# Optimization experiments

Hardware: AMD Instinct MI355X
Metric: run time of the kernel (lower is better)

Reference implementation:

```python
import math
import jax, jax.numpy as jnp
import numpy as np

EMBED_DIM = 1024
NUM_HEADS = 16
HEAD_DIM = EMBED_DIM // NUM_HEADS


def setup_inputs() -> dict:
    key = jax.random.key(0)
    kx, kqkv, kproj = jax.random.split(key, 3)
    b, sq, h = 2, 2048, EMBED_DIM
    x = jax.random.normal(kx, (b, sq, h), dtype=jnp.float32)
    # torch Linear weights are [out_features, in_features]
    # xavier_uniform for qkv: bound = sqrt(6/(fan_in+fan_out))
    bound_qkv = math.sqrt(6.0 / (h + 3 * h))
    Wqkv = jax.random.uniform(kqkv, (3 * h, h), dtype=jnp.float32,
                              minval=-bound_qkv, maxval=bound_qkv)
    # kaiming_uniform(a=sqrt(5)) for proj: bound = 1/sqrt(fan_in)
    bound_p = 1.0 / math.sqrt(h)
    Wproj = jax.random.uniform(kproj, (h, h), dtype=jnp.float32,
                               minval=-bound_p, maxval=bound_p)
    bproj = jnp.zeros((h,), dtype=jnp.float32)
    # self-attention: query == key == value (module asserts equality)
    return {"query": x, "key": x, "value": x,
            "Wqkv": Wqkv, "Wproj": Wproj, "bproj": bproj}


def reference(query, key, value, Wqkv, Wproj, bproj):
    b, sq, h = query.shape
    nh, hn = NUM_HEADS, HEAD_DIM
    # permute to [sq, b, h] then flatten tokens (seq-major)
    x = jnp.transpose(query, (1, 0, 2)).reshape(sq * b, h)
    qkv = x @ Wqkv.T                       # [sq*b, 3h] (no qkv bias: add_bias_kv=False)
    qkv = qkv.reshape(sq, b, nh, 3 * hn)
    q, k, v = jnp.split(qkv, 3, axis=-1)   # each [sq, b, nh, hn]
    # view to (sq, b*nh, hn) then transpose(0,1) -> [b*nh, sq, hn] (b-major, nh-minor)
    q = q.reshape(sq, b * nh, hn).transpose(1, 0, 2)
    k = k.reshape(sq, b * nh, hn).transpose(1, 0, 2)
    v = v.reshape(sq, b * nh, hn).transpose(1, 0, 2)
    scale = 1.0 / math.sqrt(hn)
    scores = jnp.einsum('nqd,nkd->nqk', q, k) * scale   # [b*nh, sq, sq] full matrix
    attn = jax.nn.softmax(scores, axis=-1)
    ctx = jnp.einsum('nqk,nkd->nqd', attn, v)           # [b*nh, sq, hn]
    # NOTE: original code views the b*nh (b-major) dim as (nh, b) -- reproduce exactly
    ctx = ctx.reshape(nh, b, sq, hn)
    ctx = jnp.transpose(ctx, (2, 1, 0, 3)).reshape(sq * b, h)
    out = ctx @ Wproj.T + bproj
    out = out.reshape(sq, b, h)
    return jnp.transpose(out, (1, 0, 2))   # [b, sq, h]
```

## Files before the change

### kernel.cpp

```cpp
#include <hip/hip_runtime.h>
#include <stdint.h>

#define B_   2
#define SQ   2048
#define H    1024
#define NH   16
#define HN   64
#define T_TOK 4096
#define N3H  3072

typedef __bf16 bf16x8 __attribute__((ext_vector_type(8)));
typedef float  f32x4  __attribute__((ext_vector_type(4)));
typedef float  f32x16 __attribute__((ext_vector_type(16)));

#define MFMA16(a, b, c) __builtin_amdgcn_mfma_f32_16x16x32_bf16((a), (b), (c), 0, 0, 0)
#define MFMA32(a, b, c) __builtin_amdgcn_mfma_f32_32x32x16_bf16((a), (b), (c), 0, 0, 0)

#define LGKM_DRAIN() do { \
  __builtin_amdgcn_s_waitcnt(0xC07F); \
  __builtin_amdgcn_wave_barrier(); \
} while (0)

__device__ __forceinline__ uint16_t f2bf_u(float f) {
  union { float f; uint32_t u; } v; v.f = f;
  uint32_t u = v.u;
  u += 0x7fffu + ((u >> 16) & 1u);
  return (uint16_t)(u >> 16);
}

__device__ __forceinline__ uint32_t cvtpk2(float a, float b, float* sum) {
  union { __bf16 h[2]; uint32_t u; } r;
  r.h[0] = (__bf16)a;
  r.h[1] = (__bf16)b;
  *sum += (float)r.h[0] + (float)r.h[1];
  return r.u;
}

__device__ __forceinline__ bf16x8 ldb8(const uint16_t* p) {
  return *reinterpret_cast<const bf16x8*>(p);
}

__device__ __forceinline__ void gll16(const uint16_t* g, uint16_t* l) {
  __builtin_amdgcn_global_load_lds(
      (const __attribute__((address_space(1))) uint32_t*)g,
      (__attribute__((address_space(3))) uint32_t*)l, 16, 0, 0);
}

__global__ __launch_bounds__(256) void convert_kernel(
    const float* __restrict__ x, const float* __restrict__ wqkv,
    const float* __restrict__ wproj,
    uint16_t* __restrict__ xb, uint16_t* __restrict__ wqkvb,
    uint16_t* __restrict__ wprojb) {
  const int XT4 = (T_TOK * H) / 4;
  const int WQ4 = (N3H * H) / 4;
  int i4 = blockIdx.x * 256 + threadIdx.x;
  const float* src;
  uint16_t* dst;
  if (i4 < XT4) {
    int i = i4 * 4;
    int t = i >> 10, c = i & 1023;
    int bi = t & 1, s = t >> 1;
    src = x + (bi * SQ + s) * H + c;
    dst = xb + i;
  } else if (i4 < XT4 + WQ4) {
    int j = (i4 - XT4) * 4;
    src = wqkv + j; dst = wqkvb + j;
  } else {
    int j = (i4 - XT4 - WQ4) * 4;
    src = wproj + j; dst = wprojb + j;
  }
  float4 v = *(const float4*)src;
  ushort4 o;
  o.x = f2bf_u(v.x); o.y = f2bf_u(v.y); o.z = f2bf_u(v.z); o.w = f2bf_u(v.w);
  *(ushort4*)dst = o;
}

__global__ __launch_bounds__(256) void gemm_qkv_kernel(
    const uint16_t* __restrict__ xb, const uint16_t* __restrict__ wb,
    uint16_t* __restrict__ Qb, uint16_t* __restrict__ Kb,
    uint16_t* __restrict__ Vtb) {
  const int lane = threadIdx.x & 63;
  const int wave = threadIdx.x >> 6;
  const int quad = lane >> 4, l16 = lane & 15;
  const int wm = wave >> 1, wn = wave & 1;
  const int row0 = blockIdx.y * 128, col0 = blockIdx.x * 128;

  __shared__ __align__(16) char smem[4 * 64 * 76 * 2];
  uint16_t* sA = (uint16_t*)smem;
  uint16_t* sB = (uint16_t*)(smem + 8192);
  uint16_t* W  = (uint16_t*)(smem) + wave * (64 * 76);

  const int lrow = lane >> 2;
  const int lk   = (lane & 3) * 8;

  f32x4 acc[4][4];
#pragma unroll
  for (int i = 0; i < 4; ++i)
#pragma unroll
    for (int j = 0; j < 4; ++j) acc[i][j] = (f32x4){0.f, 0.f, 0.f, 0.f};

  for (int k0 = 0; k0 < H; k0 += 32) {
#pragma unroll
    for (int c = 0; c < 2; ++c) {
      int g = c * 4 + wave;
      gll16(xb + (size_t)(row0 + g * 16 + lrow) * H + k0 + lk, sA + g * 512);
      gll16(wb + (size_t)(col0 + g * 16 + lrow) * H + k0 + lk, sB + g * 512);
    }
    __syncthreads();
    bf16x8 af[4], bfr[4];
#pragma unroll
    for (int mt = 0; mt < 4; ++mt)
      af[mt] = ldb8(sA + (wm * 64 + mt * 16 + l16) * 32 + quad * 8);
#pragma unroll
    for (int nt = 0; nt < 4; ++nt)
      bfr[nt] = ldb8(sB + (wn * 64 + nt * 16 + l16) * 32 + quad * 8);
#pragma unroll
    for (int mt = 0; mt < 4; ++mt)
#pragma unroll
      for (int nt = 0; nt < 4; ++nt)
        acc[mt][nt] = MFMA16(af[mt], bfr[nt], acc[mt][nt]);
    __syncthreads();
  }

  const int c0 = col0 + wn * 64;
  const int cm = c0 >> 6;
  const int hd = cm / 3;
  const int which = cm - hd * 3;
  const int t0 = row0 + wm * 64;

  if (which < 2) {
#pragma unroll
    for (int mt = 0; mt < 4; ++mt)
#pragma unroll
      for (int nt = 0; nt < 4; ++nt)
#pragma unroll
        for (int r = 0; r < 4; ++r)
          W[(mt * 16 + quad * 4 + r) * 76 + nt * 16 + l16] = f2bf_u(acc[mt][nt][r]);
    LGKM_DRAIN();
    uint16_t* dstb = (which == 0) ? Qb : Kb;
    const int t8 = lane >> 3, d0 = (lane & 7) * 8;
#pragma unroll
    for (int it = 0; it < 8; ++it) {
      int tl = it * 8 + t8;
      int t = t0 + tl;
      int s = t >> 1;
      int n = (t & 1) * NH + hd;
      bf16x8 vv = ldb8(W + tl * 76 + d0);
      *(bf16x8*)(dstb + (size_t)(n * SQ + s) * HN + d0) = vv;
    }
  } else {
    uint32_t* W32 = (uint32_t*)W;
#pragma unroll
    for (int mt = 0; mt < 4; ++mt)
#pragma unroll
      for (int nt = 0; nt < 4; ++nt) {
        int base = (nt * 16 + l16) * 76 + mt * 8 + quad * 2;
        W32[base >> 1] =
            (uint32_t)f2bf_u(acc[mt][nt][0]) | ((uint32_t)f2bf_u(acc[mt][nt][2]) << 16);
        W32[(base >> 1) + 16] =
            (uint32_t)f2bf_u(acc[mt][nt][1]) | ((uint32_t)f2bf_u(acc[mt][nt][3]) << 16);
      }
    LGKM_DRAIN();
    const int dl = lane >> 3;
    const int bi = (lane >> 2) & 1;
    const int sc = (lane & 3) * 8;
    const int s0 = (row0 >> 1) + wm * 32;
    const int n = bi * NH + hd;
#pragma unroll
    for (int it = 0; it < 8; ++it) {
      int d = it * 8 + dl;
      bf16x8 vv = ldb8(W + d * 76 + bi * 32 + sc);
      *(bf16x8*)(Vtb + (size_t)(n * HN + d) * SQ + s0 + sc) = vv;
    }
  }
}

__global__ __launch_bounds__(512, 4) void attn_kernel(
    const uint16_t* __restrict__ Qb, const uint16_t* __restrict__ Kb,
    const uint16_t* __restrict__ Vtb, uint16_t* __restrict__ ctxb) {
  const int lane = threadIdx.x & 63;
  const int wave = threadIdx.x >> 6;
  const int l32 = lane & 31;
  const int hi  = lane >> 5;
  const int wq = wave & 3;
  const int hf = wave >> 2;

  const int bid = blockIdx.x;
  const int xcd = bid & 7, slot = bid >> 3;
  const int head = xcd * 4 + (slot >> 4);
  const int qt   = slot & 15;
  const int q0w  = qt * 128 + wq * 32;

  const uint16_t* Qh = Qb + (size_t)head * SQ * HN;
  const uint16_t* Kh = Kb + (size_t)head * SQ * HN;
  const uint16_t* Vh = Vtb + (size_t)head * HN * SQ;

  __shared__ __align__(16) char smem[65536];
  float (*cacc)[64][33] = (float(*)[64][33])smem;
  uint16_t* ctile = (uint16_t*)(smem + 36864) + wq * (32 * 72);

  const int lr8 = lane >> 3, lc8 = lane & 7;
  const int sc8 = (lc8 - lr8) & 7;

  bf16x8 qf[4];
#pragma unroll
  for (int dc = 0; dc < 4; ++dc)
    qf[dc] = ldb8(Qh + (size_t)(q0w + l32) * HN + dc * 16 + hi * 8);

  f32x16 acc[2];
#pragma unroll
  for (int dt = 0; dt < 2; ++dt)
#pragma unroll
    for (int e = 0; e < 16; ++e) acc[dt][e] = 0.f;
  float lrun = 0.f;
  const float sc2 = 0.125f * 1.44269504f;

  auto STAGE = [&](int b, int kt) {
    uint16_t* sK = (uint16_t*)(smem + hf * 32768 + b * 16384);
    uint16_t* sV = sK + 4096;
    const int kbase = (hf * 16 + kt) * 64;
#pragma unroll
    for (int j = 0; j < 2; ++j) {
      int rr = wq * 16 + j * 8;
      gll16(Kh + (size_t)(kbase + rr + lr8) * HN + sc8 * 8, sK + rr * 64);
      gll16(Vh + (size_t)(rr + lr8) * SQ + kbase + sc8 * 8, sV + rr * 64);
    }
  };

  STAGE(0, 0);
  __syncthreads();

#pragma unroll 2
  for (int kt = 0; kt < 16; ++kt) {
    const int cur = kt & 1;
    if (kt < 15) STAGE(cur ^ 1, kt + 1);
    const uint16_t* sK = (const uint16_t*)(smem + hf * 32768 + cur * 16384);
    const uint16_t* sV = sK + 4096;

#pragma unroll
    for (int ktile = 0; ktile < 2; ++ktile) {
      f32x16 s;
#pragma unroll
      for (int e = 0; e < 16; ++e) s[e] = 0.f;
#pragma unroll
      for (int dc = 0; dc < 4; ++dc) {
        bf16x8 kf = ldb8(sK + (ktile * 32 + l32) * 64 + ((dc * 2 + hi + l32) & 7) * 8);
        s = MFMA32(kf, qf[dc], s);
      }
      uint32_t c[8];
#pragma unroll
      for (int i = 0; i < 8; ++i) {
        float p0 = __builtin_amdgcn_exp2f(s[2 * i] * sc2);
        float p1 = __builtin_amdgcn_exp2f(s[2 * i + 1] * sc2);
        c[i] = cvtpk2(p0, p1, &lrun);
      }
      uint32_t w[8];
#pragma unroll
      for (int g = 0; g < 2; ++g)
#pragma unroll
        for (int x = 0; x < 2; ++x) {
          uint32_t a  = c[g * 4 + x];
          uint32_t bb = c[g * 4 + 2 + x];
          uint32_t ta = (uint32_t)__shfl_xor((int)a, 32);
          uint32_t tb = (uint32_t)__shfl_xor((int)bb, 32);
          w[g * 4 + x]     = hi ? tb : a;
          w[g * 4 + 2 + x] = hi ? bb : ta;
        }
      union { uint32_t u[4]; bf16x8 v; } pa0, pa1;
#pragma unroll
      for (int x = 0; x < 4; ++x) { pa0.u[x] = w[x]; pa1.u[x] = w[4 + x]; }
#pragma unroll
      for (int dt = 0; dt < 2; ++dt) {
        bf16x8 v0 = ldb8(sV + (dt * 32 + l32) * 64 + ((ktile * 4 + 0 + hi + l32) & 7) * 8);
        bf16x8 v1 = ldb8(sV + (dt * 32 + l32) * 64 + ((ktile * 4 + 2 + hi + l32) & 7) * 8);
        acc[dt] = MFMA32(pa0.v, v0, acc[dt]);
        acc[dt] = MFMA32(pa1.v, v1, acc[dt]);
      }
    }
    __syncthreads();
  }

  if (hf) {
    float* dst = &cacc[wq][lane][0];
#pragma unroll
    for (int dt = 0; dt < 2; ++dt)
#pragma unroll
      for (int e = 0; e < 16; ++e) dst[dt * 16 + e] = acc[dt][e];
    dst[32] = lrun;
  }
  __syncthreads();
  if (hf) return;
  {
    const float* src = &cacc[wq][lane][0];
#pragma unroll
    for (int dt = 0; dt < 2; ++dt)
#pragma unroll
      for (int e = 0; e < 16; ++e) acc[dt][e] += src[dt * 16 + e];
    lrun += src[32];
  }

  float ls = lrun + __shfl_xor(lrun, 32);
  float rinv = __builtin_amdgcn_rcpf(ls);
#pragma unroll
  for (int e = 0; e < 16; ++e) {
    int qe = (e & 3) + 8 * (e >> 2) + 4 * hi;
    float rv = __shfl(rinv, qe);
    ctile[qe * 72 + l32]      = f2bf_u(acc[0][e] * rv);
    ctile[qe * 72 + 32 + l32] = f2bf_u(acc[1][e] * rv);
  }
  LGKM_DRAIN();
  {
    const int q8 = lane >> 3, d0 = (lane & 7) * 8;
    const int gcb = (head >> 1) * HN;
#pragma unroll
    for (int it = 0; it < 4; ++it) {
      int ql = it * 8 + q8;
      bf16x8 vv = ldb8(ctile + ql * 72 + d0);
      int row = 2 * (q0w + ql) + (head & 1);
      *(bf16x8*)(ctxb + (size_t)row * H + gcb + d0) = vv;
    }
  }
}

__global__ __launch_bounds__(256) void gemm_proj_kernel(
    const uint16_t* __restrict__ ab, const uint16_t* __restrict__ wb,
    const float* __restrict__ bias, float* __restrict__ out) {
  const int lane = threadIdx.x & 63;
  const int wave = threadIdx.x >> 6;
  const int quad = lane >> 4, l16 = lane & 15;
  const int row0 = blockIdx.y * 128, col0 = blockIdx.x * 64;

  __shared__ __align__(16) uint16_t sA[128 * 32];
  __shared__ __align__(16) uint16_t sB[64 * 32];

  const int lrow = lane >> 2;
  const int lk   = (lane & 3) * 8;

  f32x4 acc[2][4];
#pragma unroll
  for (int i = 0; i < 2; ++i)
#pragma unroll
    for (int j = 0; j < 4; ++j) acc[i][j] = (f32x4){0.f, 0.f, 0.f, 0.f};

  for (int k0 = 0; k0 < H; k0 += 32) {
#pragma unroll
    for (int c = 0; c < 2; ++c) {
      int g = c * 4 + wave;
      gll16(ab + (size_t)(row0 + g * 16 + lrow) * H + k0 + lk, sA + g * 512);
    }
    gll16(wb + (size_t)(col0 + wave * 16 + lrow) * H + k0 + lk, sB + wave * 512);
    __syncthreads();
    bf16x8 af[2], bfr[4];
#pragma unroll
    for (int mt = 0; mt < 2; ++mt)
      af[mt] = ldb8(sA + (wave * 32 + mt * 16 + l16) * 32 + quad * 8);
#pragma unroll
    for (int nt = 0; nt < 4; ++nt)
      bfr[nt] = ldb8(sB + (nt * 16 + l16) * 32 + quad * 8);
#pragma unroll
    for (int mt = 0; mt < 2; ++mt)
#pragma unroll
      for (int nt = 0; nt < 4; ++nt)
        acc[mt][nt] = MFMA16(af[mt], bfr[nt], acc[mt][nt]);
    __syncthreads();
  }

#pragma unroll
  for (int mt = 0; mt < 2; ++mt)
#pragma unroll
    for (int nt = 0; nt < 4; ++nt)
#pragma unroll
      for (int r = 0; r < 4; ++r) {
        int m = row0 + wave * 32 + mt * 16 + quad * 4 + r;
        int c = col0 + nt * 16 + l16;
        int s = m >> 1, bi = m & 1;
        out[(size_t)(bi * SQ + s) * H + c] = acc[mt][nt][r] + bias[c];
      }
}

extern "C" void kernel_launch(void* const* d_in, const int* in_sizes, int n_in,
                              void* d_out, int out_size, void* d_ws, size_t ws_size,
                              hipStream_t stream) {
  const float* x     = (const float*)d_in[0];
  const float* wqkv  = (const float*)d_in[3];
  const float* wproj = (const float*)d_in[4];
  const float* bproj = (const float*)d_in[5];
  float* out = (float*)d_out;

  char* ws = (char*)d_ws;
  uint16_t* xb     = (uint16_t*)(ws);
  uint16_t* wqkvb  = (uint16_t*)(ws + (8ull  << 20));
  uint16_t* wprojb = (uint16_t*)(ws + (14ull << 20));
  uint16_t* Qb     = (uint16_t*)(ws + (16ull << 20));
  uint16_t* Kb     = (uint16_t*)(ws + (24ull << 20));
  uint16_t* Vtb    = (uint16_t*)(ws + (32ull << 20));
  uint16_t* ctxb   = (uint16_t*)(ws + (40ull << 20));

  convert_kernel<<<8192, 256, 0, stream>>>(x, wqkv, wproj, xb, wqkvb, wprojb);
  gemm_qkv_kernel<<<dim3(N3H / 128, T_TOK / 128), 256, 0, stream>>>(xb, wqkvb, Qb, Kb, Vtb);
  attn_kernel<<<512, 512, 0, stream>>>(Qb, Kb, Vtb, ctxb);
  gemm_proj_kernel<<<dim3(H / 64, T_TOK / 128), 256, 0, stream>>>(ctxb, wprojb, bproj, out);
}
```

Measured before the change: 216.3 us.

## Fold softmax scale into Q, drop KV split, permute V to skip shuffles

The QKV GEMM epilogue now multiplies Q by scale*log2e, so the attention loop can call exp2 directly with no per-element multiply. The V transpose store permutes the sequence order within each 16-wide group, which lets the P fragment feed the PV MFMA without cross-lane shuffles. The attention block shrinks from 512 to 256 threads and each wave now covers all 32 key tiles instead of half, which removes the LDS reduction across the two halves. The row sum uses fp32 probabilities rather than the rounded bf16 values, and s_setprio is raised around the MFMA sections. The trade-off is half the waves per block, a longer serial loop per wave and less parallelism across keys.

```diff
diff --git a/kernel.cpp b/kernel.cpp
--- a/kernel.cpp
+++ b/kernel.cpp
@@ -28,11 +28,10 @@
   return (uint16_t)(u >> 16);
 }
 
-__device__ __forceinline__ uint32_t cvtpk2(float a, float b, float* sum) {
+__device__ __forceinline__ uint32_t pk2(float a, float b) {
   union { __bf16 h[2]; uint32_t u; } r;
   r.h[0] = (__bf16)a;
   r.h[1] = (__bf16)b;
-  *sum += (float)r.h[0] + (float)r.h[1];
   return r.u;
 }
 
@@ -129,13 +128,14 @@
   const int t0 = row0 + wm * 64;
 
   if (which < 2) {
+    const float qs = (which == 0) ? 0.18033688f : 1.0f;
 #pragma unroll
     for (int mt = 0; mt < 4; ++mt)
 #pragma unroll
       for (int nt = 0; nt < 4; ++nt)
 #pragma unroll
         for (int r = 0; r < 4; ++r)
-          W[(mt * 16 + quad * 4 + r) * 76 + nt * 16 + l16] = f2bf_u(acc[mt][nt][r]);
+          W[(mt * 16 + quad * 4 + r) * 76 + nt * 16 + l16] = f2bf_u(acc[mt][nt][r] * qs);
     LGKM_DRAIN();
     uint16_t* dstb = (which == 0) ? Qb : Kb;
     const int t8 = lane >> 3, d0 = (lane & 7) * 8;
@@ -166,38 +166,39 @@
     const int sc = (lane & 3) * 8;
     const int s0 = (row0 >> 1) + wm * 32;
     const int n = bi * NH + hd;
+    const int sb = sc & ~15;
+    const int hh = (sc >> 3) & 1;
 #pragma unroll
     for (int it = 0; it < 8; ++it) {
       int d = it * 8 + dl;
-      bf16x8 vv = ldb8(W + d * 76 + bi * 32 + sc);
-      *(bf16x8*)(Vtb + (size_t)(n * HN + d) * SQ + s0 + sc) = vv;
-    }
-  }
-}
-
-__global__ __launch_bounds__(512, 4) void attn_kernel(
+      const uint16_t* Wr = W + d * 76 + bi * 32 + sb + hh * 4;
+      union { uint64_t q[2]; bf16x8 v; } vv;
+      vv.q[0] = *(const uint64_t*)(Wr);
+      vv.q[1] = *(const uint64_t*)(Wr + 8);
+      *(bf16x8*)(Vtb + (size_t)(n * HN + d) * SQ + s0 + sc) = vv.v;
+    }
+  }
+}
+
+__global__ __launch_bounds__(256, 5) void attn_kernel(
     const uint16_t* __restrict__ Qb, const uint16_t* __restrict__ Kb,
     const uint16_t* __restrict__ Vtb, uint16_t* __restrict__ ctxb) {
   const int lane = threadIdx.x & 63;
   const int wave = threadIdx.x >> 6;
   const int l32 = lane & 31;
   const int hi  = lane >> 5;
-  const int wq = wave & 3;
-  const int hf = wave >> 2;
 
   const int bid = blockIdx.x;
   const int xcd = bid & 7, slot = bid >> 3;
   const int head = xcd * 4 + (slot >> 4);
   const int qt   = slot & 15;
-  const int q0w  = qt * 128 + wq * 32;
+  const int q0w  = qt * 128 + wave * 32;
 
   const uint16_t* Qh = Qb + (size_t)head * SQ * HN;
   const uint16_t* Kh = Kb + (size_t)head * SQ * HN;
   const uint16_t* Vh = Vtb + (size_t)head * HN * SQ;
 
-  __shared__ __align__(16) char smem[65536];
-  float (*cacc)[64][33] = (float(*)[64][33])smem;
-  uint16_t* ctile = (uint16_t*)(smem + 36864) + wq * (32 * 72);
+  __shared__ __align__(16) char smem[32768];
 
   const int lr8 = lane >> 3, lc8 = lane & 7;
   const int sc8 = (lc8 - lr8) & 7;
@@ -213,15 +214,14 @@
 #pragma unroll
     for (int e = 0; e < 16; ++e) acc[dt][e] = 0.f;
   float lrun = 0.f;
-  const float sc2 = 0.125f * 1.44269504f;
 
   auto STAGE = [&](int b, int kt) {
-    uint16_t* sK = (uint16_t*)(smem + hf * 32768 + b * 16384);
+    uint16_t* sK = (uint16_t*)(smem + b * 16384);
     uint16_t* sV = sK + 4096;
-    const int kbase = (hf * 16 + kt) * 64;
+    const int kbase = kt * 64;
 #pragma unroll
     for (int j = 0; j < 2; ++j) {
-      int rr = wq * 16 + j * 8;
+      int rr = wave * 16 + j * 8;
       gll16(Kh + (size_t)(kbase + rr + lr8) * HN + sc8 * 8, sK + rr * 64);
       gll16(Vh + (size_t)(rr + lr8) * SQ + kbase + sc8 * 8, sV + rr * 64);
     }
@@ -231,10 +231,10 @@
   __syncthreads();
 
 #pragma unroll 2
-  for (int kt = 0; kt < 16; ++kt) {
+  for (int kt = 0; kt < 32; ++kt) {
     const int cur = kt & 1;
-    if (kt < 15) STAGE(cur ^ 1, kt + 1);
-    const uint16_t* sK = (const uint16_t*)(smem + hf * 32768 + cur * 16384);
+    if (kt < 31) STAGE(cur ^ 1, kt + 1);
+    const uint16_t* sK = (const uint16_t*)(smem + cur * 16384);
     const uint16_t* sV = sK + 4096;
 
 #pragma unroll
@@ -242,33 +242,26 @@
       f32x16 s;
 #pragma unroll
       for (int e = 0; e < 16; ++e) s[e] = 0.f;
+      __builtin_amdgcn_s_setprio(1);
 #pragma unroll
       for (int dc = 0; dc < 4; ++dc) {
         bf16x8 kf = ldb8(sK + (ktile * 32 + l32) * 64 + ((dc * 2 + hi + l32) & 7) * 8);
         s = MFMA32(kf, qf[dc], s);
       }
+      __builtin_amdgcn_s_setprio(0);
       uint32_t c[8];
 #pragma unroll
       for (int i = 0; i < 8; ++i) {
-        float p0 = __builtin_amdgcn_exp2f(s[2 * i] * sc2);
-        float p1 = __builtin_amdgcn_exp2f(s[2 * i + 1] * sc2);
-        c[i] = cvtpk2(p0, p1, &lrun);
-      }
-      uint32_t w[8];
-#pragma unroll
-      for (int g = 0; g < 2; ++g)
-#pragma unroll
-        for (int x = 0; x < 2; ++x) {
-          uint32_t a  = c[g * 4 + x];
-          uint32_t bb = c[g * 4 + 2 + x];
-          uint32_t ta = (uint32_t)__shfl_xor((int)a, 32);
-          uint32_t tb = (uint32_t)__shfl_xor((int)bb, 32);
-          w[g * 4 + x]     = hi ? tb : a;
-          w[g * 4 + 2 + x] = hi ? bb : ta;
-        }
+        float p0 = __builtin_amdgcn_exp2f(s[2 * i]);
+        float p1 = __builtin_amdgcn_exp2f(s[2 * i + 1]);
+        lrun += p0;
+        lrun += p1;
+        c[i] = pk2(p0, p1);
+      }
       union { uint32_t u[4]; bf16x8 v; } pa0, pa1;
 #pragma unroll
-      for (int x = 0; x < 4; ++x) { pa0.u[x] = w[x]; pa1.u[x] = w[4 + x]; }
+      for (int x = 0; x < 4; ++x) { pa0.u[x] = c[x]; pa1.u[x] = c[4 + x]; }
+      __builtin_amdgcn_s_setprio(1);
 #pragma unroll
       for (int dt = 0; dt < 2; ++dt) {
         bf16x8 v0 = ldb8(sV + (dt * 32 + l32) * 64 + ((ktile * 4 + 0 + hi + l32) & 7) * 8);
@@ -276,31 +269,14 @@
         acc[dt] = MFMA32(pa0.v, v0, acc[dt]);
         acc[dt] = MFMA32(pa1.v, v1, acc[dt]);
       }
-    }
-    __syncthreads();
-  }
-
-  if (hf) {
-    float* dst = &cacc[wq][lane][0];
-#pragma unroll
-    for (int dt = 0; dt < 2; ++dt)
-#pragma unroll
-      for (int e = 0; e < 16; ++e) dst[dt * 16 + e] = acc[dt][e];
-    dst[32] = lrun;
-  }
-  __syncthreads();
-  if (hf) return;
-  {
-    const float* src = &cacc[wq][lane][0];
-#pragma unroll
-    for (int dt = 0; dt < 2; ++dt)
-#pragma unroll
-      for (int e = 0; e < 16; ++e) acc[dt][e] += src[dt * 16 + e];
-    lrun += src[32];
+      __builtin_amdgcn_s_setprio(0);
+    }
+    __syncthreads();
   }
 
   float ls = lrun + __shfl_xor(lrun, 32);
   float rinv = __builtin_amdgcn_rcpf(ls);
+  uint16_t* ctile = (uint16_t*)smem + wave * (32 * 72);
 #pragma unroll
   for (int e = 0; e < 16; ++e) {
     int qe = (e & 3) + 8 * (e >> 2) + 4 * hi;
@@ -398,6 +374,6 @@
 
   convert_kernel<<<8192, 256, 0, stream>>>(x, wqkv, wproj, xb, wqkvb, wprojb);
   gemm_qkv_kernel<<<dim3(N3H / 128, T_TOK / 128), 256, 0, stream>>>(xb, wqkvb, Qb, Kb, Vtb);
-  attn_kernel<<<512, 512, 0, stream>>>(Qb, Kb, Vtb, ctxb);
+  attn_kernel<<<512, 256, 0, stream>>>(Qb, Kb, Vtb, ctxb);
   gemm_proj_kernel<<<dim3(H / 64, T_TOK / 128), 256, 0, stream>>>(ctxb, wprojb, bproj, out);
 }
```

After: 264.5 us. +22.3%, slower.
